# Kernel optimization log

Measured on AMD Instinct MI355X. Metric: run time of the kernel, lower is better.

Reference implementation:

```python
import jax, jax.numpy as jnp
import numpy as np

NEG_INF = -jnp.inf


def setup_inputs() -> dict:
    key = jax.random.key(0)
    k1, k2, k3 = jax.random.split(key, 3)
    b, d, n_classes = 8192, 512, 100
    x = jax.random.normal(k1, (b, d), dtype=jnp.float32)
    y = jax.random.randint(k2, (b,), 0, n_classes, dtype=jnp.int64)
    T = jax.random.uniform(k3, (), dtype=jnp.float32)
    return {"x": x, "y": y, "T": T}


def reference(x, y, T):
    b = x.shape[0]
    # normalize by (unbiased, like torch) std of the whole tensor
    xs = x / jnp.std(x, ddof=1)
    # pairwise euclidean distance via gram matrix: ||xi-xj||^2 = ni + nj - 2 xi.xj
    sqn = jnp.sum(xs * xs, axis=1)                      # [b]
    sqd = sqn[:, None] + sqn[None, :] - 2.0 * (xs @ xs.T)  # [b, b]
    sqd = jnp.maximum(sqd, 0.0)
    eye = jnp.eye(b, dtype=bool)
    # diagonal is masked out later; replace 0 with 1 before sqrt for safe grads
    dist = jnp.sqrt(jnp.where(eye, 1.0, sqd))           # [b, b]
    e_dist = -dist * jnp.power(10.0, T)                 # [b, b]
    # denominator: all pairs except self
    den_dist = jnp.where(eye, NEG_INF, e_dist)
    # numerator: same-label pairs except self (inv=False)
    same = (y[:, None] == y[None, :]) & (~eye)
    num_dist = jnp.where(same, e_dist, NEG_INF)
    num = jax.nn.logsumexp(num_dist, axis=1)            # [b]
    den = jax.nn.logsumexp(den_dist, axis=1)            # [b]
    # rows with no positives (num = -inf) are zeroed out, as in the torch code
    bad = jnp.isinf(num)
    num = jnp.where(bad, 0.0, num)
    den = jnp.where(bad, 0.0, den)
    return -jnp.mean(num - den)
```

## Files before the change

### kernel.cpp

```cpp
#include <hip/hip_runtime.h>


#define NROW 8192
#define NDIM 512
#define BM   128
#define BK   32
#define NKT  (NDIM / BK)
#define NT   (NROW / BM)
#define NBLK (NT * (NT + 1) / 2)

typedef __attribute__((ext_vector_type(8))) short bf16x8;
typedef __attribute__((ext_vector_type(4))) float f32x4;

#define NEG_INF (-__builtin_inff())

static const size_t WS_SCAL = 4096;
static const size_t WS_XB   = 8192;
static const size_t WS_SQN  = WS_XB + (size_t)NROW * NDIM * 2;
static const size_t WS_RS   = WS_SQN + (size_t)NROW * 4;
static const size_t WS_P4   = WS_RS + (size_t)NROW * 4;

__device__ __forceinline__ unsigned short f2bf(float f) {
    unsigned int u = __float_as_uint(f);
    u += 0x7FFFu + ((u >> 16) & 1u);
    return (unsigned short)(u >> 16);
}

#define GLD_LDS16(gp, lp) __builtin_amdgcn_global_load_lds( \
    (const __attribute__((address_space(1))) unsigned int*)(gp), \
    (__attribute__((address_space(3))) unsigned int*)(lp), 16, 0, 0)

__global__ __launch_bounds__(256) void k_norm(const float* __restrict__ x,
                                              unsigned short* __restrict__ xb,
                                              float* __restrict__ sqn,
                                              float* __restrict__ rsum) {
    int w = threadIdx.x >> 6, lane = threadIdx.x & 63;
    int row = blockIdx.x * 4 + w;
    const float4* xr = (const float4*)(x + (size_t)row * NDIM);
    ushort4* xo = (ushort4*)(xb + (size_t)row * NDIM);
    float ss = 0.f, s1 = 0.f;
#pragma unroll
    for (int ph = 0; ph < 2; ++ph) {
        float4 v = xr[ph * 64 + lane];
        ss += v.x * v.x + v.y * v.y + v.z * v.z + v.w * v.w;
        s1 += (v.x + v.y) + (v.z + v.w);
        xo[ph * 64 + lane] = make_ushort4(f2bf(v.x), f2bf(v.y), f2bf(v.z), f2bf(v.w));
    }
#pragma unroll
    for (int off = 32; off >= 1; off >>= 1) {
        ss += __shfl_xor(ss, off, 64);
        s1 += __shfl_xor(s1, off, 64);
    }
    if (lane == 0) { sqn[row] = ss; rsum[row] = s1; }
}

__global__ __launch_bounds__(256) void k_prep(const float* __restrict__ sqn,
                                              const float* __restrict__ rsum,
                                              float* __restrict__ scal,
                                              float* __restrict__ out) {
    int t = threadIdx.x;
    double s = 0.0, ss = 0.0;
    for (int i = t; i < NROW; i += 256) { s += (double)rsum[i]; ss += (double)sqn[i]; }
#pragma unroll
    for (int off = 32; off >= 1; off >>= 1) {
        s  += __shfl_xor(s, off, 64);
        ss += __shfl_xor(ss, off, 64);
    }
    __shared__ double sa[4], sb[4];
    int w = t >> 6, lane = t & 63;
    if (lane == 0) { sa[w] = s; sb[w] = ss; }
    __syncthreads();
    if (t == 0) {
        double S = sa[0] + sa[1] + sa[2] + sa[3];
        double SS = sb[0] + sb[1] + sb[2] + sb[3];
        const double N = (double)NROW * (double)NDIM;
        double var = (SS - S * S / N) / (N - 1.0);
        scal[0] = (float)(1.0 / sqrt(var));
        out[0] = 0.f;
    }
}

__global__ __launch_bounds__(256, 3) void k_main(const unsigned short* __restrict__ xb,
                                                 const float* __restrict__ sqn,
                                                 const int* __restrict__ y,
                                                 const float* __restrict__ Tp,
                                                 const float* __restrict__ scal,
                                                 float4* __restrict__ part) {
    __shared__ __attribute__((aligned(16))) unsigned short lds[3][2][BM * BK];
    float4* P    = (float4*)&lds[0][0][0];
    float4* redC = P + 2048;

    int bid = blockIdx.x;
    int bswz = (bid & 7) * (NBLK / 8) + (bid >> 3);
    int L = bswz, rt = 0, rem = NT;
    while (L >= rem) { L -= rem; --rem; ++rt; }
    int ct = rt + L;
    const bool diag = (rt == ct);

    const int tid = threadIdx.x;
    const int w = tid >> 6, lane = tid & 63;
    const int wr = w >> 1, wc = w & 1;
    const int g = lane >> 4, qq = lane & 15;
    const int rowTile = rt * BM, colTile = ct * BM;

    const int q0 = w * 2, q1 = w * 2 + 1;
    const int colg = ((lane & 3) ^ ((lane >> 3) & 3)) * 8;
    const int sr = lane >> 2;
    const unsigned short* gA0 = xb + (size_t)(rowTile + q0 * 16 + sr) * NDIM + colg;
    const unsigned short* gA1 = xb + (size_t)(rowTile + q1 * 16 + sr) * NDIM + colg;
    const unsigned short* gB0 = xb + (size_t)(colTile + q0 * 16 + sr) * NDIM + colg;
    const unsigned short* gB1 = xb + (size_t)(colTile + q1 * 16 + sr) * NDIM + colg;

#define STAGE_T(buf, ke) do { \
    GLD_LDS16(gA0 + (ke), &lds[buf][0][q0 * 512]); \
    GLD_LDS16(gA1 + (ke), &lds[buf][0][q1 * 512]); \
    GLD_LDS16(gB0 + (ke), &lds[buf][1][q0 * 512]); \
    GLD_LDS16(gB1 + (ke), &lds[buf][1][q1 * 512]); } while (0)

    const int kx = (g ^ ((qq >> 1) & 3)) * 8;
    const int aoff = (wr * 64 + qq) * BK + kx;
    const int boff = (wc * 64 + qq) * BK + kx;

    f32x4 acc[4][4];
    const f32x4 zero = {0.f, 0.f, 0.f, 0.f};
#pragma unroll
    for (int i = 0; i < 4; ++i)
#pragma unroll
        for (int j = 0; j < 4; ++j) acc[i][j] = zero;

    STAGE_T(0, 0);
    STAGE_T(1, BK);

    int c = 0;
    for (int kt = 0; kt < NKT; ++kt) {
        if (kt + 2 < NKT) {
            int sb = c + 2; if (sb >= 3) sb -= 3;
            STAGE_T(sb, (kt + 2) * BK);
            asm volatile("s_waitcnt vmcnt(8)" ::: "memory");
        } else if (kt + 1 < NKT) {
            asm volatile("s_waitcnt vmcnt(4)" ::: "memory");
        } else {
            asm volatile("s_waitcnt vmcnt(0)" ::: "memory");
        }
        __builtin_amdgcn_s_barrier();

        const unsigned short* AA = &lds[c][0][0];
        const unsigned short* BB = &lds[c][1][0];
        bf16x8 af[4], bfr[4];
#pragma unroll
        for (int mi = 0; mi < 4; ++mi)
            af[mi] = *(const bf16x8*)&AA[aoff + mi * 16 * BK];
#pragma unroll
        for (int ni = 0; ni < 4; ++ni)
            bfr[ni] = *(const bf16x8*)&BB[boff + ni * 16 * BK];
        __builtin_amdgcn_s_setprio(1);
#pragma unroll
        for (int mi = 0; mi < 4; ++mi)
#pragma unroll
            for (int ni = 0; ni < 4; ++ni)
                acc[mi][ni] = __builtin_amdgcn_mfma_f32_16x16x32_bf16(
                    af[mi], bfr[ni], acc[mi][ni], 0, 0, 0);
        __builtin_amdgcn_s_setprio(0);
        asm volatile("s_waitcnt lgkmcnt(0)" ::: "memory");
        __builtin_amdgcn_s_barrier();
        c += 1; if (c == 3) c = 0;
    }

    const float c2 = scal[0] * __builtin_amdgcn_exp2f(Tp[0] * 3.321928094887362f)
                             * 1.4426950408889634f;
    float scol[4]; int ycol[4];
#pragma unroll
    for (int ni = 0; ni < 4; ++ni) {
        int C = colTile + wc * 64 + ni * 16 + qq;
        scol[ni] = sqn[C];
        ycol[ni] = y[C];
    }

    unsigned mm0 = 0, mm1 = 0;
#pragma unroll
    for (int mi = 0; mi < 4; ++mi) {
        float srow4[4]; int yrow4[4];
#pragma unroll
        for (int r = 0; r < 4; ++r) {
            int R = rowTile + wr * 64 + mi * 16 + g * 4 + r;
            srow4[r] = sqn[R];
            yrow4[r] = y[R];
        }
#pragma unroll
        for (int r = 0; r < 4; ++r) {
            const int R = rowTile + wr * 64 + mi * 16 + g * 4 + r;
#pragma unroll
            for (int ni = 0; ni < 4; ++ni) {
                const int C = colTile + wc * 64 + ni * 16 + qq;
                float sq = fmaf(-2.f, acc[mi][ni][r], srow4[r] + scol[ni]);
                sq = fmaxf(sq, 0.f);
                float s2 = -__builtin_amdgcn_sqrtf(sq) * c2;
                if (R == C) s2 = NEG_INF;
                acc[mi][ni][r] = s2;
                unsigned bit = (yrow4[r] == ycol[ni]) ? 1u : 0u;
                int idx = ((mi & 1) * 4 + r) * 4 + ni;
                if (mi < 2) mm0 |= bit << idx; else mm1 |= bit << idx;
            }
        }
    }

    if (!diag) {
#pragma unroll
        for (int ni = 0; ni < 4; ++ni) {
            float mx = NEG_INF;
#pragma unroll
            for (int mi = 0; mi < 4; ++mi)
#pragma unroll
                for (int r = 0; r < 4; ++r) mx = fmaxf(mx, acc[mi][ni][r]);
            mx = fmaxf(mx, __shfl_xor(mx, 16, 64));
            mx = fmaxf(mx, __shfl_xor(mx, 32, 64));
            float ld = 0.f, ln = 0.f;
#pragma unroll
            for (int mi = 0; mi < 4; ++mi) {
                unsigned mmw = (mi < 2) ? mm0 : mm1;
#pragma unroll
                for (int r = 0; r < 4; ++r) {
                    float e = __builtin_amdgcn_exp2f(acc[mi][ni][r] - mx);
                    ld += e;
                    ln += ((mmw >> (((mi & 1) * 4 + r) * 4 + ni)) & 1) ? e : 0.f;
                }
            }
            ld += __shfl_xor(ld, 16, 64); ld += __shfl_xor(ld, 32, 64);
            ln += __shfl_xor(ln, 16, 64); ln += __shfl_xor(ln, 32, 64);
            if (g == 0) {
                int lc = wc * 64 + ni * 16 + qq;
                redC[lc * 2 + wr] = make_float4(mx, ld, ln, 0.f);
            }
        }
    }

#define ROW_WRITE                                                           \
#pragma unroll                                                              \
        for (int mi = 0; mi < 4; ++mi) {                                    \
            unsigned mmw = (mi < 2) ? mm0 : mm1;                            \
_Pragma("unroll")                                                           \
            for (int r = 0; r < 4; ++r) {                                   \
                float m_l = fmaxf(fmaxf(acc[mi][0][r], acc[mi][1][r]),      \
                                  fmaxf(acc[mi][2][r], acc[mi][3][r]));     \
                float ld = 0.f, ln = 0.f;                                   \
_Pragma("unroll")                                                           \
                for (int ni = 0; ni < 4; ++ni) {                            \
                    float e = __builtin_amdgcn_exp2f(acc[mi][ni][r] - m_l); \
                    ld += e;                                                \
                    ln += ((mmw >> (((mi & 1) * 4 + r) * 4 + ni)) & 1) ? e : 0.f; \
                }                                                           \
                int lr = mi * 16 + g * 4 + r;                               \
                P[(wc * 16 + qq) * 64 + (lr ^ qq)] = make_float4(m_l, ld, ln, 0.f); \
            }                                                               \
        }

    if (wr == 0) {
#pragma unroll
        for (int mi = 0; mi < 4; ++mi) {
            unsigned mmw = (mi < 2) ? mm0 : mm1;
#pragma unroll
            for (int r = 0; r < 4; ++r) {
                float m_l = fmaxf(fmaxf(acc[mi][0][r], acc[mi][1][r]),
                                  fmaxf(acc[mi][2][r], acc[mi][3][r]));
                float ld = 0.f, ln = 0.f;
#pragma unroll
                for (int ni = 0; ni < 4; ++ni) {
                    float e = __builtin_amdgcn_exp2f(acc[mi][ni][r] - m_l);
                    ld += e;
                    ln += ((mmw >> (((mi & 1) * 4 + r) * 4 + ni)) & 1) ? e : 0.f;
                }
                int lr = mi * 16 + g * 4 + r;
                P[(wc * 16 + qq) * 64 + (lr ^ qq)] = make_float4(m_l, ld, ln, 0.f);
            }
        }
    }
    __syncthreads();
    if (w == 0) {
        float M = NEG_INF, Ls = 0.f, Ln = 0.f;
#pragma unroll
        for (int wcx = 0; wcx < 2; ++wcx)
#pragma unroll
            for (int q = 0; q < 16; ++q) {
                float4 p = P[(wcx * 16 + q) * 64 + (lane ^ q)];
                if (p.x > M) {
                    float s = __builtin_amdgcn_exp2f(M - p.x);
                    Ls *= s; Ln *= s; M = p.x;
                }
                float e = __builtin_amdgcn_exp2f(p.x - M);
                Ls += p.y * e; Ln += p.z * e;
            }
        part[(size_t)ct * NROW + rowTile + lane] = make_float4(M, Ls, Ln, 0.f);
    }
    __syncthreads();
    if (wr == 1) {
#pragma unroll
        for (int mi = 0; mi < 4; ++mi) {
            unsigned mmw = (mi < 2) ? mm0 : mm1;
#pragma unroll
            for (int r = 0; r < 4; ++r) {
                float m_l = fmaxf(fmaxf(acc[mi][0][r], acc[mi][1][r]),
                                  fmaxf(acc[mi][2][r], acc[mi][3][r]));
                float ld = 0.f, ln = 0.f;
#pragma unroll
                for (int ni = 0; ni < 4; ++ni) {
                    float e = __builtin_amdgcn_exp2f(acc[mi][ni][r] - m_l);
                    ld += e;
                    ln += ((mmw >> (((mi & 1) * 4 + r) * 4 + ni)) & 1) ? e : 0.f;
                }
                int lr = mi * 16 + g * 4 + r;
                P[(wc * 16 + qq) * 64 + (lr ^ qq)] = make_float4(m_l, ld, ln, 0.f);
            }
        }
    }
    __syncthreads();
    if (w == 2) {
        float M = NEG_INF, Ls = 0.f, Ln = 0.f;
#pragma unroll
        for (int wcx = 0; wcx < 2; ++wcx)
#pragma unroll
            for (int q = 0; q < 16; ++q) {
                float4 p = P[(wcx * 16 + q) * 64 + (lane ^ q)];
                if (p.x > M) {
                    float s = __builtin_amdgcn_exp2f(M - p.x);
                    Ls *= s; Ln *= s; M = p.x;
                }
                float e = __builtin_amdgcn_exp2f(p.x - M);
                Ls += p.y * e; Ln += p.z * e;
            }
        part[(size_t)ct * NROW + rowTile + 64 + lane] = make_float4(M, Ls, Ln, 0.f);
    }
    if (!diag) {
        __syncthreads();
        if (tid < BM) {
            float4 a = redC[tid * 2 + 0], b = redC[tid * 2 + 1];
            float M = fmaxf(a.x, b.x);
            float e0 = __builtin_amdgcn_exp2f(a.x - M), e1 = __builtin_amdgcn_exp2f(b.x - M);
            part[(size_t)rt * NROW + colTile + tid] =
                make_float4(M, a.y * e0 + b.y * e1, a.z * e0 + b.z * e1, 0.f);
        }
    }
#undef STAGE_T
}

__global__ __launch_bounds__(256) void k_rows(const float4* __restrict__ part,
                                              float* __restrict__ out) {
    int r = blockIdx.x * 256 + threadIdx.x;
    float M = NEG_INF, Ls = 0.f, Ln = 0.f;
    for (int ctt = 0; ctt < NT; ++ctt) {
        float4 p = part[(size_t)ctt * NROW + r];
        if (p.x > M) {
            float sc = __builtin_amdgcn_exp2f(M - p.x);
            Ls *= sc; Ln *= sc; M = p.x;
        }
        float s2 = __builtin_amdgcn_exp2f(p.x - M);
        Ls += p.y * s2;
        Ln += p.z * s2;
    }
    float v = (Ln > 0.f) ? (__builtin_amdgcn_logf(Ln) - __builtin_amdgcn_logf(Ls))
                               * 0.69314718055994530942f
                         : 0.f;
#pragma unroll
    for (int off = 32; off >= 1; off >>= 1) v += __shfl_xor(v, off, 64);
    __shared__ float sa[4];
    int w = threadIdx.x >> 6, lane = threadIdx.x & 63;
    if (lane == 0) sa[w] = v;
    __syncthreads();
    if (threadIdx.x == 0)
        atomicAdd(out, -((sa[0] + sa[1] + sa[2] + sa[3]) / (float)NROW));
}

extern "C" void kernel_launch(void* const* d_in, const int* in_sizes, int n_in,
                              void* d_out, int out_size, void* d_ws, size_t ws_size,
                              hipStream_t stream) {
    (void)in_sizes; (void)n_in; (void)out_size; (void)ws_size;
    const float* x  = (const float*)d_in[0];
    const int*   y  = (const int*)d_in[1];
    const float* Tp = (const float*)d_in[2];
    float* out = (float*)d_out;

    char* ws = (char*)d_ws;
    float*          scal = (float*)(ws + WS_SCAL);
    unsigned short* xb   = (unsigned short*)(ws + WS_XB);
    float*          sqn  = (float*)(ws + WS_SQN);
    float*          rsum = (float*)(ws + WS_RS);
    float4*         p4   = (float4*)(ws + WS_P4);

    k_norm <<<NROW / 4, 256, 0, stream>>>(x, xb, sqn, rsum);
    k_prep <<<1, 256, 0, stream>>>(sqn, rsum, scal, out);
    k_main <<<NBLK, 256, 0, stream>>>(xb, sqn, y, Tp, scal, p4);
    k_rows <<<NROW / 256, 256, 0, stream>>>(p4, out);
}
```

Baseline: 98.81 us.

## Shrink LDS to double buffering and alias epilogue scratch to raise occupancy

Replaces the triple-buffered LDS staging (48 KB) with a 32 KB double-buffered arena and raises launch bounds from 3 to 5 blocks per CU. Row reductions now run first, and the column reduction scratch (redC) aliases the same arena behind an extra barrier. The goal is more resident waves to hide latency, at the cost of one fewer prefetch stage and tighter register limits that may cause spills.

```diff
diff --git a/kernel.cpp b/kernel.cpp
--- a/kernel.cpp
+++ b/kernel.cpp
@@ -8,6 +8,7 @@
 #define NKT  (NDIM / BK)
 #define NT   (NROW / BM)
 #define NBLK (NT * (NT + 1) / 2)
+#define TILE (BM * BK)
 
 typedef __attribute__((ext_vector_type(8))) short bf16x8;
 typedef __attribute__((ext_vector_type(4))) float f32x4;
@@ -80,15 +81,16 @@
     }
 }
 
-__global__ __launch_bounds__(256, 3) void k_main(const unsigned short* __restrict__ xb,
+__global__ __launch_bounds__(256, 5) void k_main(const unsigned short* __restrict__ xb,
                                                  const float* __restrict__ sqn,
                                                  const int* __restrict__ y,
                                                  const float* __restrict__ Tp,
                                                  const float* __restrict__ scal,
                                                  float4* __restrict__ part) {
-    __shared__ __attribute__((aligned(16))) unsigned short lds[3][2][BM * BK];
-    float4* P    = (float4*)&lds[0][0][0];
-    float4* redC = P + 2048;
+    __shared__ __attribute__((aligned(16))) unsigned char arena[32768];
+    unsigned short* stag = (unsigned short*)arena;
+    float4* P    = (float4*)arena;
+    float4* redC = (float4*)arena;
 
     int bid = blockIdx.x;
     int bswz = (bid & 7) * (NBLK / 8) + (bid >> 3);
@@ -112,10 +114,10 @@
     const unsigned short* gB1 = xb + (size_t)(colTile + q1 * 16 + sr) * NDIM + colg;
 
 #define STAGE_T(buf, ke) do { \
-    GLD_LDS16(gA0 + (ke), &lds[buf][0][q0 * 512]); \
-    GLD_LDS16(gA1 + (ke), &lds[buf][0][q1 * 512]); \
-    GLD_LDS16(gB0 + (ke), &lds[buf][1][q0 * 512]); \
-    GLD_LDS16(gB1 + (ke), &lds[buf][1][q1 * 512]); } while (0)
+    GLD_LDS16(gA0 + (ke), stag + ((buf) * 2 + 0) * TILE + q0 * 512); \
+    GLD_LDS16(gA1 + (ke), stag + ((buf) * 2 + 0) * TILE + q1 * 512); \
+    GLD_LDS16(gB0 + (ke), stag + ((buf) * 2 + 1) * TILE + q0 * 512); \
+    GLD_LDS16(gB1 + (ke), stag + ((buf) * 2 + 1) * TILE + q1 * 512); } while (0)
 
     const int kx = (g ^ ((qq >> 1) & 3)) * 8;
     const int aoff = (wr * 64 + qq) * BK + kx;
@@ -129,23 +131,19 @@
         for (int j = 0; j < 4; ++j) acc[i][j] = zero;
 
     STAGE_T(0, 0);
-    STAGE_T(1, BK);
-
-    int c = 0;
+
     for (int kt = 0; kt < NKT; ++kt) {
-        if (kt + 2 < NKT) {
-            int sb = c + 2; if (sb >= 3) sb -= 3;
-            STAGE_T(sb, (kt + 2) * BK);
-            asm volatile("s_waitcnt vmcnt(8)" ::: "memory");
-        } else if (kt + 1 < NKT) {
+        const int c = kt & 1;
+        if (kt + 1 < NKT) {
+            STAGE_T(c ^ 1, (kt + 1) * BK);
             asm volatile("s_waitcnt vmcnt(4)" ::: "memory");
         } else {
             asm volatile("s_waitcnt vmcnt(0)" ::: "memory");
         }
         __builtin_amdgcn_s_barrier();
 
-        const unsigned short* AA = &lds[c][0][0];
-        const unsigned short* BB = &lds[c][1][0];
+        const unsigned short* AA = stag + (c * 2 + 0) * TILE;
+        const unsigned short* BB = stag + (c * 2 + 1) * TILE;
         bf16x8 af[4], bfr[4];
 #pragma unroll
         for (int mi = 0; mi < 4; ++mi)
@@ -163,7 +161,6 @@
         __builtin_amdgcn_s_setprio(0);
         asm volatile("s_waitcnt lgkmcnt(0)" ::: "memory");
         __builtin_amdgcn_s_barrier();
-        c += 1; if (c == 3) c = 0;
     }
 
     const float c2 = scal[0] * __builtin_amdgcn_exp2f(Tp[0] * 3.321928094887362f)
@@ -204,7 +201,84 @@
         }
     }
 
+    if (wr == 0) {
+#pragma unroll
+        for (int mi = 0; mi < 4; ++mi) {
+            unsigned mmw = (mi < 2) ? mm0 : mm1;
+#pragma unroll
+            for (int r = 0; r < 4; ++r) {
+                float m_l = fmaxf(fmaxf(acc[mi][0][r], acc[mi][1][r]),
+                                  fmaxf(acc[mi][2][r], acc[mi][3][r]));
+                float ld = 0.f, ln = 0.f;
+#pragma unroll
+                for (int ni = 0; ni < 4; ++ni) {
+                    float e = __builtin_amdgcn_exp2f(acc[mi][ni][r] - m_l);
+                    ld += e;
+                    ln += ((mmw >> (((mi & 1) * 4 + r) * 4 + ni)) & 1) ? e : 0.f;
+                }
+                int lr = mi * 16 + g * 4 + r;
+                P[(wc * 16 + qq) * 64 + (lr ^ qq)] = make_float4(m_l, ld, ln, 0.f);
+            }
+        }
+    }
+    __syncthreads();
+    if (w == 0) {
+        float M = NEG_INF, Ls = 0.f, Ln = 0.f;
+#pragma unroll
+        for (int wcx = 0; wcx < 2; ++wcx)
+#pragma unroll
+            for (int q = 0; q < 16; ++q) {
+                float4 p = P[(wcx * 16 + q) * 64 + (lane ^ q)];
+                if (p.x > M) {
+                    float s = __builtin_amdgcn_exp2f(M - p.x);
+                    Ls *= s; Ln *= s; M = p.x;
+                }
+                float e = __builtin_amdgcn_exp2f(p.x - M);
+                Ls += p.y * e; Ln += p.z * e;
+            }
+        part[(size_t)ct * NROW + rowTile + lane] = make_float4(M, Ls, Ln, 0.f);
+    }
+    __syncthreads();
+    if (wr == 1) {
+#pragma unroll
+        for (int mi = 0; mi < 4; ++mi) {
+            unsigned mmw = (mi < 2) ? mm0 : mm1;
+#pragma unroll
+            for (int r = 0; r < 4; ++r) {
+                float m_l = fmaxf(fmaxf(acc[mi][0][r], acc[mi][1][r]),
+                                  fmaxf(acc[mi][2][r], acc[mi][3][r]));
+                float ld = 0.f, ln = 0.f;
+#pragma unroll
+                for (int ni = 0; ni < 4; ++ni) {
+                    float e = __builtin_amdgcn_exp2f(acc[mi][ni][r] - m_l);
+                    ld += e;
+                    ln += ((mmw >> (((mi & 1) * 4 + r) * 4 + ni)) & 1) ? e : 0.f;
+                }
+                int lr = mi * 16 + g * 4 + r;
+                P[(wc * 16 + qq) * 64 + (lr ^ qq)] = make_float4(m_l, ld, ln, 0.f);
+            }
+        }
+    }
+    __syncthreads();
+    if (w == 2) {
+        float M = NEG_INF, Ls = 0.f, Ln = 0.f;
+#pragma unroll
+        for (int wcx = 0; wcx < 2; ++wcx)
+#pragma unroll
+            for (int q = 0; q < 16; ++q) {
+                float4 p = P[(wcx * 16 + q) * 64 + (lane ^ q)];
+                if (p.x > M) {
+                    float s = __builtin_amdgcn_exp2f(M - p.x);
+                    Ls *= s; Ln *= s; M = p.x;
+                }
+                float e = __builtin_amdgcn_exp2f(p.x - M);
+                Ls += p.y * e; Ln += p.z * e;
+            }
+        part[(size_t)ct * NROW + rowTile + 64 + lane] = make_float4(M, Ls, Ln, 0.f);
+    }
+
     if (!diag) {
+        __syncthreads();
 #pragma unroll
         for (int ni = 0; ni < 4; ++ni) {
             float mx = NEG_INF;
@@ -232,104 +306,6 @@
                 redC[lc * 2 + wr] = make_float4(mx, ld, ln, 0.f);
             }
         }
-    }
-
-#define ROW_WRITE                                                           \
-#pragma unroll                                                              \
-        for (int mi = 0; mi < 4; ++mi) {                                    \
-            unsigned mmw = (mi < 2) ? mm0 : mm1;                            \
-_Pragma("unroll")                                                           \
-            for (int r = 0; r < 4; ++r) {                                   \
-                float m_l = fmaxf(fmaxf(acc[mi][0][r], acc[mi][1][r]),      \
-                                  fmaxf(acc[mi][2][r], acc[mi][3][r]));     \
-                float ld = 0.f, ln = 0.f;                                   \
-_Pragma("unroll")                                                           \
-                for (int ni = 0; ni < 4; ++ni) {                            \
-                    float e = __builtin_amdgcn_exp2f(acc[mi][ni][r] - m_l); \
-                    ld += e;                                                \
-                    ln += ((mmw >> (((mi & 1) * 4 + r) * 4 + ni)) & 1) ? e : 0.f; \
-                }                                                           \
-                int lr = mi * 16 + g * 4 + r;                               \
-                P[(wc * 16 + qq) * 64 + (lr ^ qq)] = make_float4(m_l, ld, ln, 0.f); \
-            }                                                               \
-        }
-
-    if (wr == 0) {
-#pragma unroll
-        for (int mi = 0; mi < 4; ++mi) {
-            unsigned mmw = (mi < 2) ? mm0 : mm1;
-#pragma unroll
-            for (int r = 0; r < 4; ++r) {
-                float m_l = fmaxf(fmaxf(acc[mi][0][r], acc[mi][1][r]),
-                                  fmaxf(acc[mi][2][r], acc[mi][3][r]));
-                float ld = 0.f, ln = 0.f;
-#pragma unroll
-                for (int ni = 0; ni < 4; ++ni) {
-                    float e = __builtin_amdgcn_exp2f(acc[mi][ni][r] - m_l);
-                    ld += e;
-                    ln += ((mmw >> (((mi & 1) * 4 + r) * 4 + ni)) & 1) ? e : 0.f;
-                }
-                int lr = mi * 16 + g * 4 + r;
-                P[(wc * 16 + qq) * 64 + (lr ^ qq)] = make_float4(m_l, ld, ln, 0.f);
-            }
-        }
-    }
-    __syncthreads();
-    if (w == 0) {
-        float M = NEG_INF, Ls = 0.f, Ln = 0.f;
-#pragma unroll
-        for (int wcx = 0; wcx < 2; ++wcx)
-#pragma unroll
-            for (int q = 0; q < 16; ++q) {
-                float4 p = P[(wcx * 16 + q) * 64 + (lane ^ q)];
-                if (p.x > M) {
-                    float s = __builtin_amdgcn_exp2f(M - p.x);
-                    Ls *= s; Ln *= s; M = p.x;
-                }
-                float e = __builtin_amdgcn_exp2f(p.x - M);
-                Ls += p.y * e; Ln += p.z * e;
-            }
-        part[(size_t)ct * NROW + rowTile + lane] = make_float4(M, Ls, Ln, 0.f);
-    }
-    __syncthreads();
-    if (wr == 1) {
-#pragma unroll
-        for (int mi = 0; mi < 4; ++mi) {
-            unsigned mmw = (mi < 2) ? mm0 : mm1;
-#pragma unroll
-            for (int r = 0; r < 4; ++r) {
-                float m_l = fmaxf(fmaxf(acc[mi][0][r], acc[mi][1][r]),
-                                  fmaxf(acc[mi][2][r], acc[mi][3][r]));
-                float ld = 0.f, ln = 0.f;
-#pragma unroll
-                for (int ni = 0; ni < 4; ++ni) {
-                    float e = __builtin_amdgcn_exp2f(acc[mi][ni][r] - m_l);
-                    ld += e;
-                    ln += ((mmw >> (((mi & 1) * 4 + r) * 4 + ni)) & 1) ? e : 0.f;
-                }
-                int lr = mi * 16 + g * 4 + r;
-                P[(wc * 16 + qq) * 64 + (lr ^ qq)] = make_float4(m_l, ld, ln, 0.f);
-            }
-        }
-    }
-    __syncthreads();
-    if (w == 2) {
-        float M = NEG_INF, Ls = 0.f, Ln = 0.f;
-#pragma unroll
-        for (int wcx = 0; wcx < 2; ++wcx)
-#pragma unroll
-            for (int q = 0; q < 16; ++q) {
-                float4 p = P[(wcx * 16 + q) * 64 + (lane ^ q)];
-                if (p.x > M) {
-                    float s = __builtin_amdgcn_exp2f(M - p.x);
-                    Ls *= s; Ln *= s; M = p.x;
-                }
-                float e = __builtin_amdgcn_exp2f(p.x - M);
-                Ls += p.y * e; Ln += p.z * e;
-            }
-        part[(size_t)ct * NROW + rowTile + 64 + lane] = make_float4(M, Ls, Ln, 0.f);
-    }
-    if (!diag) {
         __syncthreads();
         if (tid < BM) {
             float4 a = redC[tid * 2 + 0], b = redC[tid * 2 + 1];
```

Result: slower. 354.1 us (+258.4%).

## Remap triangular tile order into 8x8 super-tiles and reorder epilogue reductions

Applied to the files above, without the earlier changes.

Replaces the row-major walk over upper-triangular tile pairs with a super-tile ordering: a group of 8x8 tiles is enumerated as its diagonal triangle followed by off-diagonal 8x8 blocks. Consecutive blocks then share row and column panels, which should improve L2 reuse of the bf16 operands. The epilogue is also reordered so the row reductions run before the column reduction, with an added barrier guarding the LDS reuse of redC. Mapping correctness depends on the hard-coded constants (36, 64, 8) matching NT=64.

```diff
diff --git a/kernel.cpp b/kernel.cpp
--- a/kernel.cpp
+++ b/kernel.cpp
@@ -8,6 +8,7 @@
 #define NKT  (NDIM / BK)
 #define NT   (NROW / BM)
 #define NBLK (NT * (NT + 1) / 2)
+#define TILE (BM * BK)
 
 typedef __attribute__((ext_vector_type(8))) short bf16x8;
 typedef __attribute__((ext_vector_type(4))) float f32x4;
@@ -86,15 +87,24 @@
                                                  const float* __restrict__ Tp,
                                                  const float* __restrict__ scal,
                                                  float4* __restrict__ part) {
-    __shared__ __attribute__((aligned(16))) unsigned short lds[3][2][BM * BK];
+    __shared__ __attribute__((aligned(16))) unsigned short lds[3][2][TILE];
     float4* P    = (float4*)&lds[0][0][0];
     float4* redC = P + 2048;
 
     int bid = blockIdx.x;
-    int bswz = (bid & 7) * (NBLK / 8) + (bid >> 3);
-    int L = bswz, rt = 0, rem = NT;
-    while (L >= rem) { L -= rem; --rem; ++rt; }
-    int ct = rt + L;
+    int L = (bid & 7) * (NBLK / 8) + (bid >> 3);
+    int RT = 0;
+    for (;;) { int cnt = 36 + 64 * (7 - RT); if (L < cnt) break; L -= cnt; ++RT; }
+    int rt, ct;
+    if (L < 36) {
+        int i = 0;
+        while (L >= 8 - i) { L -= 8 - i; ++i; }
+        rt = RT * 8 + i; ct = RT * 8 + i + L;
+    } else {
+        L -= 36;
+        int CT = RT + 1 + (L >> 6), cc = L & 63;
+        rt = RT * 8 + (cc >> 3); ct = CT * 8 + (cc & 7);
+    }
     const bool diag = (rt == ct);
 
     const int tid = threadIdx.x;
@@ -204,7 +214,84 @@
         }
     }
 
+    if (wr == 0) {
+#pragma unroll
+        for (int mi = 0; mi < 4; ++mi) {
+            unsigned mmw = (mi < 2) ? mm0 : mm1;
+#pragma unroll
+            for (int r = 0; r < 4; ++r) {
+                float m_l = fmaxf(fmaxf(acc[mi][0][r], acc[mi][1][r]),
+                                  fmaxf(acc[mi][2][r], acc[mi][3][r]));
+                float ld = 0.f, ln = 0.f;
+#pragma unroll
+                for (int ni = 0; ni < 4; ++ni) {
+                    float e = __builtin_amdgcn_exp2f(acc[mi][ni][r] - m_l);
+                    ld += e;
+                    ln += ((mmw >> (((mi & 1) * 4 + r) * 4 + ni)) & 1) ? e : 0.f;
+                }
+                int lr = mi * 16 + g * 4 + r;
+                P[(wc * 16 + qq) * 64 + (lr ^ qq)] = make_float4(m_l, ld, ln, 0.f);
+            }
+        }
+    }
+    __syncthreads();
+    if (w == 0) {
+        float M = NEG_INF, Ls = 0.f, Ln = 0.f;
+#pragma unroll
+        for (int wcx = 0; wcx < 2; ++wcx)
+#pragma unroll
+            for (int q = 0; q < 16; ++q) {
+                float4 p = P[(wcx * 16 + q) * 64 + (lane ^ q)];
+                if (p.x > M) {
+                    float s = __builtin_amdgcn_exp2f(M - p.x);
+                    Ls *= s; Ln *= s; M = p.x;
+                }
+                float e = __builtin_amdgcn_exp2f(p.x - M);
+                Ls += p.y * e; Ln += p.z * e;
+            }
+        part[(size_t)ct * NROW + rowTile + lane] = make_float4(M, Ls, Ln, 0.f);
+    }
+    __syncthreads();
+    if (wr == 1) {
+#pragma unroll
+        for (int mi = 0; mi < 4; ++mi) {
+            unsigned mmw = (mi < 2) ? mm0 : mm1;
+#pragma unroll
+            for (int r = 0; r < 4; ++r) {
+                float m_l = fmaxf(fmaxf(acc[mi][0][r], acc[mi][1][r]),
+                                  fmaxf(acc[mi][2][r], acc[mi][3][r]));
+                float ld = 0.f, ln = 0.f;
+#pragma unroll
+                for (int ni = 0; ni < 4; ++ni) {
+                    float e = __builtin_amdgcn_exp2f(acc[mi][ni][r] - m_l);
+                    ld += e;
+                    ln += ((mmw >> (((mi & 1) * 4 + r) * 4 + ni)) & 1) ? e : 0.f;
+                }
+                int lr = mi * 16 + g * 4 + r;
+                P[(wc * 16 + qq) * 64 + (lr ^ qq)] = make_float4(m_l, ld, ln, 0.f);
+            }
+        }
+    }
+    __syncthreads();
+    if (w == 2) {
+        float M = NEG_INF, Ls = 0.f, Ln = 0.f;
+#pragma unroll
+        for (int wcx = 0; wcx < 2; ++wcx)
+#pragma unroll
+            for (int q = 0; q < 16; ++q) {
+                float4 p = P[(wcx * 16 + q) * 64 + (lane ^ q)];
+                if (p.x > M) {
+                    float s = __builtin_amdgcn_exp2f(M - p.x);
+                    Ls *= s; Ln *= s; M = p.x;
+                }
+                float e = __builtin_amdgcn_exp2f(p.x - M);
+                Ls += p.y * e; Ln += p.z * e;
+            }
+        part[(size_t)ct * NROW + rowTile + 64 + lane] = make_float4(M, Ls, Ln, 0.f);
+    }
+
     if (!diag) {
+        __syncthreads();
 #pragma unroll
         for (int ni = 0; ni < 4; ++ni) {
             float mx = NEG_INF;
@@ -232,104 +319,6 @@
                 redC[lc * 2 + wr] = make_float4(mx, ld, ln, 0.f);
             }
         }
-    }
-
-#define ROW_WRITE                                                           \
-#pragma unroll                                                              \
-        for (int mi = 0; mi < 4; ++mi) {                                    \
-            unsigned mmw = (mi < 2) ? mm0 : mm1;                            \
-_Pragma("unroll")                                                           \
-            for (int r = 0; r < 4; ++r) {                                   \
-                float m_l = fmaxf(fmaxf(acc[mi][0][r], acc[mi][1][r]),      \
-                                  fmaxf(acc[mi][2][r], acc[mi][3][r]));     \
-                float ld = 0.f, ln = 0.f;                                   \
-_Pragma("unroll")                                                           \
-                for (int ni = 0; ni < 4; ++ni) {                            \
-                    float e = __builtin_amdgcn_exp2f(acc[mi][ni][r] - m_l); \
-                    ld += e;                                                \
-                    ln += ((mmw >> (((mi & 1) * 4 + r) * 4 + ni)) & 1) ? e : 0.f; \
-                }                                                           \
-                int lr = mi * 16 + g * 4 + r;                               \
-                P[(wc * 16 + qq) * 64 + (lr ^ qq)] = make_float4(m_l, ld, ln, 0.f); \
-            }                                                               \
-        }
-
-    if (wr == 0) {
-#pragma unroll
-        for (int mi = 0; mi < 4; ++mi) {
-            unsigned mmw = (mi < 2) ? mm0 : mm1;
-#pragma unroll
-            for (int r = 0; r < 4; ++r) {
-                float m_l = fmaxf(fmaxf(acc[mi][0][r], acc[mi][1][r]),
-                                  fmaxf(acc[mi][2][r], acc[mi][3][r]));
-                float ld = 0.f, ln = 0.f;
-#pragma unroll
-                for (int ni = 0; ni < 4; ++ni) {
-                    float e = __builtin_amdgcn_exp2f(acc[mi][ni][r] - m_l);
-                    ld += e;
-                    ln += ((mmw >> (((mi & 1) * 4 + r) * 4 + ni)) & 1) ? e : 0.f;
-                }
-                int lr = mi * 16 + g * 4 + r;
-                P[(wc * 16 + qq) * 64 + (lr ^ qq)] = make_float4(m_l, ld, ln, 0.f);
-            }
-        }
-    }
-    __syncthreads();
-    if (w == 0) {
-        float M = NEG_INF, Ls = 0.f, Ln = 0.f;
-#pragma unroll
-        for (int wcx = 0; wcx < 2; ++wcx)
-#pragma unroll
-            for (int q = 0; q < 16; ++q) {
-                float4 p = P[(wcx * 16 + q) * 64 + (lane ^ q)];
-                if (p.x > M) {
-                    float s = __builtin_amdgcn_exp2f(M - p.x);
-                    Ls *= s; Ln *= s; M = p.x;
-                }
-                float e = __builtin_amdgcn_exp2f(p.x - M);
-                Ls += p.y * e; Ln += p.z * e;
-            }
-        part[(size_t)ct * NROW + rowTile + lane] = make_float4(M, Ls, Ln, 0.f);
-    }
-    __syncthreads();
-    if (wr == 1) {
-#pragma unroll
-        for (int mi = 0; mi < 4; ++mi) {
-            unsigned mmw = (mi < 2) ? mm0 : mm1;
-#pragma unroll
-            for (int r = 0; r < 4; ++r) {
-                float m_l = fmaxf(fmaxf(acc[mi][0][r], acc[mi][1][r]),
-                                  fmaxf(acc[mi][2][r], acc[mi][3][r]));
-                float ld = 0.f, ln = 0.f;
-#pragma unroll
-                for (int ni = 0; ni < 4; ++ni) {
-                    float e = __builtin_amdgcn_exp2f(acc[mi][ni][r] - m_l);
-                    ld += e;
-                    ln += ((mmw >> (((mi & 1) * 4 + r) * 4 + ni)) & 1) ? e : 0.f;
-                }
-                int lr = mi * 16 + g * 4 + r;
-                P[(wc * 16 + qq) * 64 + (lr ^ qq)] = make_float4(m_l, ld, ln, 0.f);
-            }
-        }
-    }
-    __syncthreads();
-    if (w == 2) {
-        float M = NEG_INF, Ls = 0.f, Ln = 0.f;
-#pragma unroll
-        for (int wcx = 0; wcx < 2; ++wcx)
-#pragma unroll
-            for (int q = 0; q < 16; ++q) {
-                float4 p = P[(wcx * 16 + q) * 64 + (lane ^ q)];
-                if (p.x > M) {
-                    float s = __builtin_amdgcn_exp2f(M - p.x);
-                    Ls *= s; Ln *= s; M = p.x;
-                }
-                float e = __builtin_amdgcn_exp2f(p.x - M);
-                Ls += p.y * e; Ln += p.z * e;
-            }
-        part[(size_t)ct * NROW + rowTile + 64 + lane] = make_float4(M, Ls, Ln, 0.f);
-    }
-    if (!diag) {
         __syncthreads();
         if (tid < BM) {
             float4 a = redC[tid * 2 + 0], b = redC[tid * 2 + 1];
```

Result: no change. 99.96 us (+1.2%).
